# Performance work log

Hardware: AMD Instinct MI355X
Metric: run time of the kernel (lower is better)

Reference implementation:

```python
import jax, jax.numpy as jnp
import numpy as np

N_ATOMS = 100000
N_BONDS = 200000
MAX_NB = 6
ATOM_FDIM = 133
BOND_FDIM = 147
HIDDEN = 512
N_MOLS = 8192
DEPTH = 5


def setup_inputs() -> dict:
    key = jax.random.key(0)
    ks = jax.random.split(key, 10)
    f_atoms = jax.random.normal(ks[0], (N_ATOMS, ATOM_FDIM), dtype=jnp.float32)
    f_bonds = jax.random.normal(ks[1], (N_BONDS, BOND_FDIM), dtype=jnp.float32)
    # fan-in scaled weights to keep activations stable through the depth loop
    W_i = jax.random.normal(ks[2], (BOND_FDIM, HIDDEN), dtype=jnp.float32) / np.sqrt(BOND_FDIM)
    W_h = jax.random.normal(ks[3], (HIDDEN, HIDDEN), dtype=jnp.float32) / np.sqrt(HIDDEN)
    W_o = jax.random.normal(ks[4], (ATOM_FDIM + HIDDEN, HIDDEN), dtype=jnp.float32) / np.sqrt(ATOM_FDIM + HIDDEN)
    b_o = jnp.zeros((HIDDEN,), dtype=jnp.float32)
    a2b = jax.random.randint(ks[5], (N_ATOMS, MAX_NB), 0, N_BONDS, dtype=jnp.int32)
    b2a = jax.random.randint(ks[6], (N_BONDS,), 0, N_ATOMS, dtype=jnp.int32)
    b2revb = jax.random.randint(ks[7], (N_BONDS,), 0, N_BONDS, dtype=jnp.int32)
    atom_to_mol = jnp.sort(jax.random.randint(ks[8], (N_ATOMS,), 0, N_MOLS, dtype=jnp.int32))
    return {"f_atoms": f_atoms, "f_bonds": f_bonds, "W_i": W_i, "W_h": W_h,
            "W_o": W_o, "b_o": b_o, "a2b": a2b, "b2a": b2a, "b2revb": b2revb,
            "atom_to_mol": atom_to_mol, "n_mols": N_MOLS}


def reference(f_atoms, f_bonds, W_i, W_h, W_o, b_o, a2b, b2a, b2revb, atom_to_mol, n_mols):
    # input = W_i(f_bonds); message = relu(input)
    inp = f_bonds @ W_i                      # [B, H]
    message = jax.nn.relu(inp)
    for _ in range(DEPTH - 1):
        nei_a_message = message[a2b]         # [A, MAX_NB, H] gather bond->atom
        a_message = nei_a_message.sum(axis=1)  # [A, H]
        message = a_message[b2a] - message[b2revb]  # [B, H]
        message = jax.nn.relu(inp + message @ W_h)  # dropout p=0 -> identity
    nei_a_message = message[a2b]             # [A, MAX_NB, H]
    a_message = nei_a_message.sum(axis=1)    # [A, H]
    a_input = jnp.concatenate([f_atoms, a_message], axis=1)  # [A, ATOM_FDIM+H]
    atom_hiddens = jax.nn.relu(a_input @ W_o + b_o)           # [A, H]
    # mean aggregation per molecule (a_scope -> segment ids)
    sums = jax.ops.segment_sum(atom_hiddens, atom_to_mol, num_segments=n_mols)
    counts = jax.ops.segment_sum(jnp.ones((atom_hiddens.shape[0],), dtype=atom_hiddens.dtype),
                                 atom_to_mol, num_segments=n_mols)
    mol_vecs = jnp.where(counts[:, None] > 0,
                         sums / jnp.maximum(counts, 1.0)[:, None],
                         jnp.zeros_like(sums))  # cached_zero_vector for empty mols
    return mol_vecs
```

## Files before the change

kernel.cpp:

```cpp
#include <hip/hip_runtime.h>
#include <hip/hip_bf16.h>
#include <cstdint>

#define A_N   100000
#define B_N   200000
#define MAXNB 6
#define AFD   133
#define BFD   147
#define HID   512
#define NMOL  8192

typedef __attribute__((ext_vector_type(8))) short bf16x8;
typedef __attribute__((ext_vector_type(4))) float f32x4;

__device__ __forceinline__ unsigned short f2b(float f) {
    unsigned u = __builtin_bit_cast(unsigned, f);
    u += 0x7fffu + ((u >> 16) & 1u);
    return (unsigned short)(u >> 16);
}
__device__ __forceinline__ float blo(unsigned u) { return __builtin_bit_cast(float, u << 16); }
__device__ __forceinline__ float bhi(unsigned u) { return __builtin_bit_cast(float, u & 0xffff0000u); }
__device__ __forceinline__ unsigned pack2f(float a, float b) {
    return (unsigned)f2b(a) | ((unsigned)f2b(b) << 16);
}
__device__ __forceinline__ void glds16(const void* g, void* l) {
    __builtin_amdgcn_global_load_lds((const __attribute__((address_space(1))) unsigned*)g,
                                     (__attribute__((address_space(3))) unsigned*)l, 16, 0, 0);
}

__global__ __launch_bounds__(256) void k_diag(float* __restrict__ out, int n, float val) {
    int i = blockIdx.x * 256 + threadIdx.x;
    if (i < n) out[i] = val;
}

__global__ __launch_bounds__(256) void k_weights(
    const float* __restrict__ Wi, const float* __restrict__ Wh, const float* __restrict__ Wo,
    unsigned short* __restrict__ WiT, unsigned short* __restrict__ WcatImg, unsigned short* __restrict__ WoT)
{
    int n = blockIdx.x, t = threadIdx.x;
    for (int k = t; k < 160; k += 256)
        WiT[(size_t)n * 160 + k] = (k < BFD) ? f2b(Wi[(size_t)k * HID + n]) : (unsigned short)0;
    for (int k = t; k < 672; k += 256) {
        unsigned short v;
        if (k < HID)             v = f2b(Wh[(size_t)k * HID + n]);
        else if (k < HID + BFD)  v = f2b(Wi[(size_t)(k - HID) * HID + n]);
        else                     v = 0;
        int row = n & 127;
        size_t tile = (size_t)(n >> 7) * 21 + (k >> 5);
        WcatImg[tile * 4096 + row * 32 + ((((k >> 3) & 3) ^ ((row >> 1) & 3)) << 3) + (k & 7)] = v;
    }
    for (int k = t; k < 672; k += 256) {
        unsigned short v;
        if (k < AFD)       v = f2b(Wo[(size_t)k * HID + n]);
        else if (k < 160)  v = 0;
        else               v = f2b(Wo[(size_t)(k - 27) * HID + n]);
        WoT[(size_t)n * 672 + k] = v;
    }
}

__global__ __launch_bounds__(256) void k_gemm_wi(
    const float* __restrict__ fb, const unsigned short* __restrict__ WiT,
    unsigned short* __restrict__ msg)
{
    __shared__ unsigned short As[128][32];
    __shared__ unsigned short Bs[128][32];
    const int orig = blockIdx.x;
    const int xcd = orig & 7, idx = orig >> 3;
    const int wg = (xcd < 4 ? xcd * 782 : 3128 + (xcd - 4) * 781) + idx;
    const int bm = wg >> 2, bn = wg & 3;
    const int row0 = bm * 128, col0 = bn * 128;

    const int tid = threadIdx.x, lane = tid & 63, wid = tid >> 6;
    const int wm = wid >> 1, wn = wid & 1;
    const int r0 = tid >> 2, c0 = tid & 3, r1 = 64 + r0;
    const int wsw = (c0 ^ ((r0 >> 1) & 3)) * 8;
    const int rsw = ((lane >> 4) ^ (((lane & 15) >> 1) & 3)) * 8;
    f32x4 acc[4][4] = {};

    const float* pf0 = fb + (size_t)min(row0 + r0, B_N - 1) * BFD;
    const float* pf1 = fb + (size_t)min(row0 + r1, B_N - 1) * BFD;
    const unsigned short* pb0 = WiT + (size_t)(col0 + r0) * 160;
    const unsigned short* pb1 = WiT + (size_t)(col0 + r1) * 160;

    float v0[8], v1[8];
    uint4 b0, b1;

#define LOADA(kt) do { int kb = (kt) * 32 + c0 * 8; \
        _Pragma("unroll") for (int i = 0; i < 8; i++) { int kg = kb + i; v0[i] = (kg < BFD) ? pf0[kg] : 0.f; } \
        _Pragma("unroll") for (int i = 0; i < 8; i++) { int kg = kb + i; v1[i] = (kg < BFD) ? pf1[kg] : 0.f; } } while (0)
#define LOADB(kt) do { int kb = (kt) * 32 + c0 * 8; \
        b0 = *(const uint4*)(pb0 + kb); b1 = *(const uint4*)(pb1 + kb); } while (0)

    LOADA(0); LOADB(0);
    for (int kt = 0; kt < 5; ++kt) {
        __syncthreads();
        uint4 q;
        q.x = pack2f(v0[0], v0[1]); q.y = pack2f(v0[2], v0[3]); q.z = pack2f(v0[4], v0[5]); q.w = pack2f(v0[6], v0[7]);
        *(uint4*)&As[r0][wsw] = q;
        q.x = pack2f(v1[0], v1[1]); q.y = pack2f(v1[2], v1[3]); q.z = pack2f(v1[4], v1[5]); q.w = pack2f(v1[6], v1[7]);
        *(uint4*)&As[r1][wsw] = q;
        *(uint4*)&Bs[r0][wsw] = b0;
        *(uint4*)&Bs[r1][wsw] = b1;
        __syncthreads();
        if (kt < 4) { LOADA(kt + 1); LOADB(kt + 1); }

        bf16x8 af[4], bfr[4];
#pragma unroll
        for (int m = 0; m < 4; m++) af[m] = *(const bf16x8*)&As[wm * 64 + m * 16 + (lane & 15)][rsw];
#pragma unroll
        for (int n = 0; n < 4; n++) bfr[n] = *(const bf16x8*)&Bs[wn * 64 + n * 16 + (lane & 15)][rsw];
#pragma unroll
        for (int m = 0; m < 4; m++)
#pragma unroll
            for (int n = 0; n < 4; n++)
                acc[m][n] = __builtin_amdgcn_mfma_f32_16x16x32_bf16(af[m], bfr[n], acc[m][n], 0, 0, 0);
    }
#undef LOADA
#undef LOADB

#pragma unroll
    for (int m = 0; m < 4; m++) {
        int rbase = row0 + wm * 64 + m * 16 + (lane >> 4) * 4;
#pragma unroll
        for (int n = 0; n < 4; n++) {
            int cg = col0 + wn * 64 + n * 16 + (lane & 15);
#pragma unroll
            for (int r = 0; r < 4; r++) {
                int rg = rbase + r;
                if (rg < B_N) {
                    float v = acc[m][n][r];
                    msg[(size_t)rg * HID + cg] = f2b(v > 0.f ? v : 0.f);
                }
            }
        }
    }
}

__global__ __launch_bounds__(256) void k_delta(
    const unsigned short* __restrict__ msg, const int* __restrict__ a2b,
    const int* __restrict__ b2a, const int* __restrict__ b2revb,
    unsigned short* __restrict__ D)
{
    int b = blockIdx.x * 4 + (threadIdx.x >> 6);
    if (b >= B_N) return;
    int lane = threadIdx.x & 63;
    const int atom = b2a[b];
    const int rev  = b2revb[b];
    const int* nb = a2b + (size_t)atom * MAXNB;
    float acc[8];
    {
        uint4 v = *(const uint4*)(msg + (size_t)rev * HID + lane * 8);
        acc[0] = -blo(v.x); acc[1] = -bhi(v.x);
        acc[2] = -blo(v.y); acc[3] = -bhi(v.y);
        acc[4] = -blo(v.z); acc[5] = -bhi(v.z);
        acc[6] = -blo(v.w); acc[7] = -bhi(v.w);
    }
#pragma unroll
    for (int k = 0; k < MAXNB; k++) {
        uint4 v = *(const uint4*)(msg + (size_t)nb[k] * HID + lane * 8);
        acc[0] += blo(v.x); acc[1] += bhi(v.x);
        acc[2] += blo(v.y); acc[3] += bhi(v.y);
        acc[4] += blo(v.z); acc[5] += bhi(v.z);
        acc[6] += blo(v.w); acc[7] += bhi(v.w);
    }
    uint4 q;
    q.x = pack2f(acc[0], acc[1]); q.y = pack2f(acc[2], acc[3]);
    q.z = pack2f(acc[4], acc[5]); q.w = pack2f(acc[6], acc[7]);
    *(uint4*)(D + (size_t)b * HID + lane * 8) = q;
}

__global__ __launch_bounds__(256, 4) void k_gemm_wh(
    const unsigned short* __restrict__ D, const float* __restrict__ fb,
    const unsigned short* __restrict__ WcatImg,
    unsigned short* __restrict__ msg_out)
{
    __shared__ unsigned short As[2][128][32];
    __shared__ unsigned short Bs[2][4096];
    const int orig = blockIdx.x;
    const int xcd = orig & 7, idx = orig >> 3;
    const int wg = (xcd < 4 ? xcd * 782 : 3128 + (xcd - 4) * 781) + idx;
    const int bm = wg >> 2, bn = wg & 3;
    const int row0 = bm * 128;

    const int tid = threadIdx.x, lane = tid & 63, wid = tid >> 6;
    const int wm = wid >> 1, wn = wid & 1;
    const int r0 = tid >> 2, c0 = tid & 3, r1 = 64 + r0;
    const int wsw = (c0 ^ ((r0 >> 1) & 3)) * 8;
    const int rsw = ((lane >> 4) ^ (((lane & 15) >> 1) & 3)) * 8;
    f32x4 acc[4][4] = {};

    const int arow1 = wid * 32 + (lane >> 2);
    const int arow2 = arow1 + 16;
    const int achk = lane & 3;
    const unsigned short* srcA1 = D + (size_t)min(row0 + arow1, B_N - 1) * HID + ((achk ^ ((arow1 >> 1) & 3)) << 3);
    const unsigned short* srcA2 = D + (size_t)min(row0 + arow2, B_N - 1) * HID + ((achk ^ ((arow2 >> 1) & 3)) << 3);
    const char* srcB = (const char*)WcatImg + (size_t)bn * 21 * 8192 + wid * 2048 + lane * 16;

    const int rg0 = min(row0 + r0, B_N - 1), rg1 = min(row0 + r1, B_N - 1);
    const float* pf0 = fb + (size_t)rg0 * BFD;
    const float* pf1 = fb + (size_t)rg1 * BFD;
    float v0[8], v1[8];

    glds16(srcA1, &As[0][wid * 32][0]);
    glds16(srcA2, &As[0][wid * 32 + 16][0]);
    glds16(srcB, &Bs[0][wid * 1024]);
    glds16(srcB + 1024, &Bs[0][wid * 1024 + 512]);

    for (int kt = 0; kt < 21; ++kt) {
        const int cur = kt & 1, nxt = cur ^ 1;
        __syncthreads();
        if (kt >= 16) {
            uint4 q;
            q.x = pack2f(v0[0], v0[1]); q.y = pack2f(v0[2], v0[3]); q.z = pack2f(v0[4], v0[5]); q.w = pack2f(v0[6], v0[7]);
            *(uint4*)&As[cur][r0][wsw] = q;
            q.x = pack2f(v1[0], v1[1]); q.y = pack2f(v1[2], v1[3]); q.z = pack2f(v1[4], v1[5]); q.w = pack2f(v1[6], v1[7]);
            *(uint4*)&As[cur][r1][wsw] = q;
            __syncthreads();
        }
        if (kt < 20) {
            if (kt + 1 < 16) {
                glds16(srcA1 + (kt + 1) * 32, &As[nxt][wid * 32][0]);
                glds16(srcA2 + (kt + 1) * 32, &As[nxt][wid * 32 + 16][0]);
            }
            glds16(srcB + (size_t)(kt + 1) * 8192, &Bs[nxt][wid * 1024]);
            glds16(srcB + (size_t)(kt + 1) * 8192 + 1024, &Bs[nxt][wid * 1024 + 512]);
        }
        if (kt >= 15 && kt < 20) {
            int kb = (kt + 1) * 32 - HID + c0 * 8;
#pragma unroll
            for (int i = 0; i < 8; i++) { int kg = kb + i; v0[i] = (kg < BFD) ? pf0[kg] : 0.f; }
#pragma unroll
            for (int i = 0; i < 8; i++) { int kg = kb + i; v1[i] = (kg < BFD) ? pf1[kg] : 0.f; }
        }
        bf16x8 af[4], bfr[4];
#pragma unroll
        for (int m = 0; m < 4; m++) af[m] = *(const bf16x8*)&As[cur][wm * 64 + m * 16 + (lane & 15)][rsw];
#pragma unroll
        for (int n = 0; n < 4; n++) bfr[n] = *(const bf16x8*)&Bs[cur][(wn * 64 + n * 16 + (lane & 15)) * 32 + rsw];
#pragma unroll
        for (int m = 0; m < 4; m++)
#pragma unroll
            for (int n = 0; n < 4; n++)
                acc[m][n] = __builtin_amdgcn_mfma_f32_16x16x32_bf16(af[m], bfr[n], acc[m][n], 0, 0, 0);
    }

#pragma unroll
    for (int m = 0; m < 4; m++) {
        int rbase = row0 + wm * 64 + m * 16 + (lane >> 4) * 4;
#pragma unroll
        for (int n = 0; n < 4; n++) {
            int cg = bn * 128 + wn * 64 + n * 16 + (lane & 15);
#pragma unroll
            for (int r = 0; r < 4; r++) {
                int rg = rbase + r;
                if (rg < B_N) {
                    float v = acc[m][n][r];
                    msg_out[(size_t)rg * HID + cg] = f2b(v > 0.f ? v : 0.f);
                }
            }
        }
    }
}

__global__ __launch_bounds__(256, 4) void k_gemm_wo(
    const float* __restrict__ fa, const unsigned short* __restrict__ amsg,
    const unsigned short* __restrict__ WoT, const float* __restrict__ bo,
    float* __restrict__ ah)
{
    __shared__ unsigned short As[2][128][32];
    __shared__ unsigned short Bs[2][128][32];
    const int orig = blockIdx.x;
    const int wg = (orig & 7) * 391 + (orig >> 3);
    const int bm = wg >> 2, bn = wg & 3;
    const int row0 = bm * 128, col0 = bn * 128;

    const int tid = threadIdx.x, lane = tid & 63, wid = tid >> 6;
    const int wm = wid >> 1, wn = wid & 1;
    const int r0 = tid >> 2, c0 = tid & 3, r1 = 64 + r0;
    const int wsw = (c0 ^ ((r0 >> 1) & 3)) * 8;
    const int rsw = ((lane >> 4) ^ (((lane & 15) >> 1) & 3)) * 8;
    f32x4 acc[4][4] = {};

    const int grow1 = wid * 32 + (lane >> 2);
    const int grow2 = grow1 + 16;
    const int gchk = lane & 3;
    const int asw1 = (gchk ^ ((grow1 >> 1) & 3)) << 3;
    const int asw2 = (gchk ^ ((grow2 >> 1) & 3)) << 3;
    const unsigned short* srcA1 = amsg + (size_t)min(row0 + grow1, A_N - 1) * HID + asw1 - 160;
    const unsigned short* srcA2 = amsg + (size_t)min(row0 + grow2, A_N - 1) * HID + asw2 - 160;
    const unsigned short* srcB1 = WoT + (size_t)(col0 + grow1) * 672 + asw1;
    const unsigned short* srcB2 = WoT + (size_t)(col0 + grow2) * 672 + asw2;

    const int rg0 = min(row0 + r0, A_N - 1), rg1 = min(row0 + r1, A_N - 1);
    const float* pf0 = fa + (size_t)rg0 * AFD;
    const float* pf1 = fa + (size_t)rg1 * AFD;
    float v0[8], v1[8];

    {
        int kb = c0 * 8;
#pragma unroll
        for (int i = 0; i < 8; i++) { int kg = kb + i; v0[i] = (kg < AFD) ? pf0[kg] : 0.f; }
#pragma unroll
        for (int i = 0; i < 8; i++) { int kg = kb + i; v1[i] = (kg < AFD) ? pf1[kg] : 0.f; }
    }
    glds16(srcB1, &Bs[0][wid * 32][0]);
    glds16(srcB2, &Bs[0][wid * 32 + 16][0]);

    for (int kt = 0; kt < 21; ++kt) {
        const int cur = kt & 1, nxt = cur ^ 1;
        __syncthreads();
        if (kt < 5) {
            uint4 q;
            q.x = pack2f(v0[0], v0[1]); q.y = pack2f(v0[2], v0[3]); q.z = pack2f(v0[4], v0[5]); q.w = pack2f(v0[6], v0[7]);
            *(uint4*)&As[cur][r0][wsw] = q;
            q.x = pack2f(v1[0], v1[1]); q.y = pack2f(v1[2], v1[3]); q.z = pack2f(v1[4], v1[5]); q.w = pack2f(v1[6], v1[7]);
            *(uint4*)&As[cur][r1][wsw] = q;
            __syncthreads();
        }
        if (kt < 20) {
            if (kt + 1 >= 5) {
                glds16(srcA1 + (kt + 1) * 32, &As[nxt][wid * 32][0]);
                glds16(srcA2 + (kt + 1) * 32, &As[nxt][wid * 32 + 16][0]);
            }
            glds16(srcB1 + (kt + 1) * 32, &Bs[nxt][wid * 32][0]);
            glds16(srcB2 + (kt + 1) * 32, &Bs[nxt][wid * 32 + 16][0]);
        }
        if (kt < 4) {
            int kb = (kt + 1) * 32 + c0 * 8;
#pragma unroll
            for (int i = 0; i < 8; i++) { int kg = kb + i; v0[i] = (kg < AFD) ? pf0[kg] : 0.f; }
#pragma unroll
            for (int i = 0; i < 8; i++) { int kg = kb + i; v1[i] = (kg < AFD) ? pf1[kg] : 0.f; }
        }
        bf16x8 af[4], bfr[4];
#pragma unroll
        for (int m = 0; m < 4; m++) af[m] = *(const bf16x8*)&As[cur][wm * 64 + m * 16 + (lane & 15)][rsw];
#pragma unroll
        for (int n = 0; n < 4; n++) bfr[n] = *(const bf16x8*)&Bs[cur][wn * 64 + n * 16 + (lane & 15)][rsw];
#pragma unroll
        for (int m = 0; m < 4; m++)
#pragma unroll
            for (int n = 0; n < 4; n++)
                acc[m][n] = __builtin_amdgcn_mfma_f32_16x16x32_bf16(af[m], bfr[n], acc[m][n], 0, 0, 0);
    }

#pragma unroll
    for (int m = 0; m < 4; m++) {
        int rbase = row0 + wm * 64 + m * 16 + (lane >> 4) * 4;
#pragma unroll
        for (int n = 0; n < 4; n++) {
            int cg = col0 + wn * 64 + n * 16 + (lane & 15);
            float bias = bo[cg];
#pragma unroll
            for (int r = 0; r < 4; r++) {
                int rg = rbase + r;
                if (rg < A_N) {
                    float v = acc[m][n][r] + bias;
                    ah[(size_t)rg * HID + cg] = v > 0.f ? v : 0.f;
                }
            }
        }
    }
}

__global__ __launch_bounds__(256) void k_gather(
    const unsigned short* __restrict__ msg, const int* __restrict__ a2b,
    unsigned short* __restrict__ amsg)
{
    int g = blockIdx.x * 4 + (threadIdx.x >> 6);
    if (g >= A_N) return;
    int lane = threadIdx.x & 63;
    const int* nb = a2b + (size_t)g * MAXNB;
    float acc[8] = {};
#pragma unroll
    for (int k = 0; k < MAXNB; k++) {
        uint4 v = *(const uint4*)(msg + (size_t)nb[k] * HID + lane * 8);
        acc[0] += blo(v.x); acc[1] += bhi(v.x);
        acc[2] += blo(v.y); acc[3] += bhi(v.y);
        acc[4] += blo(v.z); acc[5] += bhi(v.z);
        acc[6] += blo(v.w); acc[7] += bhi(v.w);
    }
    uint4 q;
    q.x = pack2f(acc[0], acc[1]); q.y = pack2f(acc[2], acc[3]);
    q.z = pack2f(acc[4], acc[5]); q.w = pack2f(acc[6], acc[7]);
    *(uint4*)(amsg + (size_t)g * HID + lane * 8) = q;
}

__global__ __launch_bounds__(256) void k_segmean(
    const float* __restrict__ ah, const int* __restrict__ a2m, float* __restrict__ out)
{
    int mol = blockIdx.x, t = threadIdx.x;
    int lo, hi;
    { int l = 0, r = A_N; while (l < r) { int m = (l + r) >> 1; if (a2m[m] < mol) l = m + 1; else r = m; } lo = l; }
    { int l = lo, r = A_N; while (l < r) { int m = (l + r) >> 1; if (a2m[m] < mol + 1) l = m + 1; else r = m; } hi = l; }
    float s0 = 0.f, s1 = 0.f;
    for (int a = lo; a < hi; a++) {
        s0 += ah[(size_t)a * HID + t];
        s1 += ah[(size_t)a * HID + 256 + t];
    }
    int c = hi - lo;
    float inv = c > 0 ? 1.0f / (float)c : 0.f;
    out[(size_t)mol * HID + t] = s0 * inv;
    out[(size_t)mol * HID + 256 + t] = s1 * inv;
}

extern "C" void kernel_launch(void* const* d_in, const int* in_sizes, int n_in,
                              void* d_out, int out_size, void* d_ws, size_t ws_size,
                              hipStream_t stream)
{
    const float* f_atoms = (const float*)d_in[0];
    const float* f_bonds = (const float*)d_in[1];
    const float* W_i     = (const float*)d_in[2];
    const float* W_h     = (const float*)d_in[3];
    const float* W_o     = (const float*)d_in[4];
    const float* b_o     = (const float*)d_in[5];
    const int*   a2b     = (const int*)d_in[6];
    const int*   b2a     = (const int*)d_in[7];
    const int*   b2revb  = (const int*)d_in[8];
    const int*   a2m     = (const int*)d_in[9];

    const size_t OFF_MSG  = 0;
    const size_t OFF_D    = 204800000;
    const size_t OFF_WIT  = 409600000;
    const size_t OFF_WCAT = 409763840;
    const size_t OFF_WOT  = 410451968;
    const size_t REQUIRED = 411140096;

    if (ws_size < REQUIRED) {
        float val = -(10000.0f + (float)(ws_size >> 20));
        k_diag<<<dim3((out_size + 255) / 256), dim3(256), 0, stream>>>((float*)d_out, out_size, val);
        return;
    }

    char* w = (char*)d_ws;
    unsigned short* msg   = (unsigned short*)(w + OFF_MSG);
    unsigned short* D     = (unsigned short*)(w + OFF_D);
    unsigned short* amsg  = (unsigned short*)(w + OFF_D);
    unsigned short* WiT   = (unsigned short*)(w + OFF_WIT);
    unsigned short* Wcat  = (unsigned short*)(w + OFF_WCAT);
    unsigned short* WoT   = (unsigned short*)(w + OFF_WOT);
    float* ah             = (float*)(w + OFF_MSG);

    k_weights<<<dim3(512), dim3(256), 0, stream>>>(W_i, W_h, W_o, WiT, Wcat, WoT);
    k_gemm_wi<<<dim3(6252), dim3(256), 0, stream>>>(f_bonds, WiT, msg);
    for (int it = 0; it < 4; ++it) {
        k_delta<<<dim3(50000), dim3(256), 0, stream>>>(msg, a2b, b2a, b2revb, D);
        k_gemm_wh<<<dim3(6252), dim3(256), 0, stream>>>(D, f_bonds, Wcat, msg);
    }
    k_gather<<<dim3(25000), dim3(256), 0, stream>>>(msg, a2b, amsg);
    k_gemm_wo<<<dim3(3128), dim3(256), 0, stream>>>(f_atoms, amsg, WoT, b_o, ah);
    k_segmean<<<dim3(NMOL), dim3(256), 0, stream>>>(ah, a2m, (float*)d_out);
}
```

Baseline: 2.384 ms.

## Widen Wh GEMM tile to 128x256 with 512 threads; batch two rows per wave in gathers

The recurrent Wh GEMM now uses 512-thread blocks computing 128x256 output tiles, so each block covers half the hidden width. This halves how many times each D row is re-read from memory, and the weight image layout is changed to 256-row tiles to match. The delta and final gather kernels now process two bonds or atoms per wavefront and issue all gather loads up front, exposing more memory-level parallelism. Costs are higher LDS and register use per block, which may lower occupancy. Both kernels also drop their bounds checks, which relies on the row counts dividing evenly.

```diff
diff --git a/kernel.cpp b/kernel.cpp
--- a/kernel.cpp
+++ b/kernel.cpp
@@ -45,9 +45,9 @@
         if (k < HID)             v = f2b(Wh[(size_t)k * HID + n]);
         else if (k < HID + BFD)  v = f2b(Wi[(size_t)(k - HID) * HID + n]);
         else                     v = 0;
-        int row = n & 127;
-        size_t tile = (size_t)(n >> 7) * 21 + (k >> 5);
-        WcatImg[tile * 4096 + row * 32 + ((((k >> 3) & 3) ^ ((row >> 1) & 3)) << 3) + (k & 7)] = v;
+        int row = n & 255;
+        size_t tile = (size_t)(n >> 8) * 21 + (k >> 5);
+        WcatImg[tile * 8192 + row * 32 + ((((k >> 3) & 3) ^ ((row >> 1) & 3)) << 3) + (k & 7)] = v;
     }
     for (int k = t; k < 672; k += 256) {
         unsigned short v;
@@ -141,68 +141,71 @@
     const int* __restrict__ b2a, const int* __restrict__ b2revb,
     unsigned short* __restrict__ D)
 {
-    int b = blockIdx.x * 4 + (threadIdx.x >> 6);
-    if (b >= B_N) return;
-    int lane = threadIdx.x & 63;
-    const int atom = b2a[b];
-    const int rev  = b2revb[b];
-    const int* nb = a2b + (size_t)atom * MAXNB;
-    float acc[8];
-    {
-        uint4 v = *(const uint4*)(msg + (size_t)rev * HID + lane * 8);
-        acc[0] = -blo(v.x); acc[1] = -bhi(v.x);
-        acc[2] = -blo(v.y); acc[3] = -bhi(v.y);
-        acc[4] = -blo(v.z); acc[5] = -bhi(v.z);
-        acc[6] = -blo(v.w); acc[7] = -bhi(v.w);
-    }
-#pragma unroll
-    for (int k = 0; k < MAXNB; k++) {
-        uint4 v = *(const uint4*)(msg + (size_t)nb[k] * HID + lane * 8);
-        acc[0] += blo(v.x); acc[1] += bhi(v.x);
-        acc[2] += blo(v.y); acc[3] += bhi(v.y);
-        acc[4] += blo(v.z); acc[5] += bhi(v.z);
-        acc[6] += blo(v.w); acc[7] += bhi(v.w);
-    }
-    uint4 q;
-    q.x = pack2f(acc[0], acc[1]); q.y = pack2f(acc[2], acc[3]);
-    q.z = pack2f(acc[4], acc[5]); q.w = pack2f(acc[6], acc[7]);
-    *(uint4*)(D + (size_t)b * HID + lane * 8) = q;
-}
-
-__global__ __launch_bounds__(256, 4) void k_gemm_wh(
+    const int base = blockIdx.x * 8 + ((threadIdx.x >> 6) << 1);
+    const int lane = threadIdx.x & 63;
+    const int bA = base, bB = base + 1;
+    const int* nbA = a2b + (size_t)b2a[bA] * MAXNB;
+    const int* nbB = a2b + (size_t)b2a[bB] * MAXNB;
+    const int revA = b2revb[bA], revB = b2revb[bB];
+    uint4 ga[7], gb[7];
+#pragma unroll
+    for (int k = 0; k < 6; k++) ga[k] = *(const uint4*)(msg + (size_t)nbA[k] * HID + lane * 8);
+    ga[6] = *(const uint4*)(msg + (size_t)revA * HID + lane * 8);
+#pragma unroll
+    for (int k = 0; k < 6; k++) gb[k] = *(const uint4*)(msg + (size_t)nbB[k] * HID + lane * 8);
+    gb[6] = *(const uint4*)(msg + (size_t)revB * HID + lane * 8);
+
+#define SUM7(g, out) do { \
+        float s[8]; \
+        s[0] = blo(g[0].x)+blo(g[1].x)+blo(g[2].x)+blo(g[3].x)+blo(g[4].x)+blo(g[5].x)-blo(g[6].x); \
+        s[1] = bhi(g[0].x)+bhi(g[1].x)+bhi(g[2].x)+bhi(g[3].x)+bhi(g[4].x)+bhi(g[5].x)-bhi(g[6].x); \
+        s[2] = blo(g[0].y)+blo(g[1].y)+blo(g[2].y)+blo(g[3].y)+blo(g[4].y)+blo(g[5].y)-blo(g[6].y); \
+        s[3] = bhi(g[0].y)+bhi(g[1].y)+bhi(g[2].y)+bhi(g[3].y)+bhi(g[4].y)+bhi(g[5].y)-bhi(g[6].y); \
+        s[4] = blo(g[0].z)+blo(g[1].z)+blo(g[2].z)+blo(g[3].z)+blo(g[4].z)+blo(g[5].z)-blo(g[6].z); \
+        s[5] = bhi(g[0].z)+bhi(g[1].z)+bhi(g[2].z)+bhi(g[3].z)+bhi(g[4].z)+bhi(g[5].z)-bhi(g[6].z); \
+        s[6] = blo(g[0].w)+blo(g[1].w)+blo(g[2].w)+blo(g[3].w)+blo(g[4].w)+blo(g[5].w)-blo(g[6].w); \
+        s[7] = bhi(g[0].w)+bhi(g[1].w)+bhi(g[2].w)+bhi(g[3].w)+bhi(g[4].w)+bhi(g[5].w)-bhi(g[6].w); \
+        out.x = pack2f(s[0], s[1]); out.y = pack2f(s[2], s[3]); \
+        out.z = pack2f(s[4], s[5]); out.w = pack2f(s[6], s[7]); } while (0)
+
+    uint4 qa, qb;
+    SUM7(ga, qa);
+    SUM7(gb, qb);
+    *(uint4*)(D + (size_t)bA * HID + lane * 8) = qa;
+    *(uint4*)(D + (size_t)bB * HID + lane * 8) = qb;
+#undef SUM7
+}
+
+__global__ __launch_bounds__(512, 4) void k_gemm_wh(
     const unsigned short* __restrict__ D, const float* __restrict__ fb,
     const unsigned short* __restrict__ WcatImg,
     unsigned short* __restrict__ msg_out)
 {
     __shared__ unsigned short As[2][128][32];
-    __shared__ unsigned short Bs[2][4096];
+    __shared__ unsigned short Bs[2][8192];
     const int orig = blockIdx.x;
     const int xcd = orig & 7, idx = orig >> 3;
-    const int wg = (xcd < 4 ? xcd * 782 : 3128 + (xcd - 4) * 781) + idx;
-    const int bm = wg >> 2, bn = wg & 3;
+    const int wg = (xcd < 6 ? xcd * 391 : 2346 + (xcd - 6) * 390) + idx;
+    const int bm = wg >> 1, bn = wg & 1;
     const int row0 = bm * 128;
 
     const int tid = threadIdx.x, lane = tid & 63, wid = tid >> 6;
-    const int wm = wid >> 1, wn = wid & 1;
-    const int r0 = tid >> 2, c0 = tid & 3, r1 = 64 + r0;
+    const int wm = wid >> 2, wn = wid & 3;
+    const int r0 = tid >> 2, c0 = tid & 3;
     const int wsw = (c0 ^ ((r0 >> 1) & 3)) * 8;
     const int rsw = ((lane >> 4) ^ (((lane & 15) >> 1) & 3)) * 8;
     f32x4 acc[4][4] = {};
 
-    const int arow1 = wid * 32 + (lane >> 2);
-    const int arow2 = arow1 + 16;
+    const int arow = wid * 16 + (lane >> 2);
     const int achk = lane & 3;
-    const unsigned short* srcA1 = D + (size_t)min(row0 + arow1, B_N - 1) * HID + ((achk ^ ((arow1 >> 1) & 3)) << 3);
-    const unsigned short* srcA2 = D + (size_t)min(row0 + arow2, B_N - 1) * HID + ((achk ^ ((arow2 >> 1) & 3)) << 3);
-    const char* srcB = (const char*)WcatImg + (size_t)bn * 21 * 8192 + wid * 2048 + lane * 16;
-
-    const int rg0 = min(row0 + r0, B_N - 1), rg1 = min(row0 + r1, B_N - 1);
-    const float* pf0 = fb + (size_t)rg0 * BFD;
-    const float* pf1 = fb + (size_t)rg1 * BFD;
-    float v0[8], v1[8];
-
-    glds16(srcA1, &As[0][wid * 32][0]);
-    glds16(srcA2, &As[0][wid * 32 + 16][0]);
+    const unsigned short* srcA = D + (size_t)min(row0 + arow, B_N - 1) * HID + ((achk ^ ((arow >> 1) & 3)) << 3);
+    const char* srcB = (const char*)WcatImg + (size_t)bn * 21 * 16384 + wid * 2048 + lane * 16;
+
+    const int rg = min(row0 + r0, B_N - 1);
+    const float* pf = fb + (size_t)rg * BFD;
+    float v0[8];
+
+    glds16(srcA, &As[0][wid * 16][0]);
     glds16(srcB, &Bs[0][wid * 1024]);
     glds16(srcB + 1024, &Bs[0][wid * 1024 + 512]);
 
@@ -213,24 +216,18 @@
             uint4 q;
             q.x = pack2f(v0[0], v0[1]); q.y = pack2f(v0[2], v0[3]); q.z = pack2f(v0[4], v0[5]); q.w = pack2f(v0[6], v0[7]);
             *(uint4*)&As[cur][r0][wsw] = q;
-            q.x = pack2f(v1[0], v1[1]); q.y = pack2f(v1[2], v1[3]); q.z = pack2f(v1[4], v1[5]); q.w = pack2f(v1[6], v1[7]);
-            *(uint4*)&As[cur][r1][wsw] = q;
             __syncthreads();
         }
         if (kt < 20) {
-            if (kt + 1 < 16) {
-                glds16(srcA1 + (kt + 1) * 32, &As[nxt][wid * 32][0]);
-                glds16(srcA2 + (kt + 1) * 32, &As[nxt][wid * 32 + 16][0]);
-            }
-            glds16(srcB + (size_t)(kt + 1) * 8192, &Bs[nxt][wid * 1024]);
-            glds16(srcB + (size_t)(kt + 1) * 8192 + 1024, &Bs[nxt][wid * 1024 + 512]);
+            if (kt + 1 < 16)
+                glds16(srcA + (kt + 1) * 32, &As[nxt][wid * 16][0]);
+            glds16(srcB + (size_t)(kt + 1) * 16384, &Bs[nxt][wid * 1024]);
+            glds16(srcB + (size_t)(kt + 1) * 16384 + 1024, &Bs[nxt][wid * 1024 + 512]);
         }
         if (kt >= 15 && kt < 20) {
             int kb = (kt + 1) * 32 - HID + c0 * 8;
 #pragma unroll
-            for (int i = 0; i < 8; i++) { int kg = kb + i; v0[i] = (kg < BFD) ? pf0[kg] : 0.f; }
-#pragma unroll
-            for (int i = 0; i < 8; i++) { int kg = kb + i; v1[i] = (kg < BFD) ? pf1[kg] : 0.f; }
+            for (int i = 0; i < 8; i++) { int kg = kb + i; v0[i] = (kg < BFD) ? pf[kg] : 0.f; }
         }
         bf16x8 af[4], bfr[4];
 #pragma unroll
@@ -249,13 +246,13 @@
         int rbase = row0 + wm * 64 + m * 16 + (lane >> 4) * 4;
 #pragma unroll
         for (int n = 0; n < 4; n++) {
-            int cg = bn * 128 + wn * 64 + n * 16 + (lane & 15);
+            int cg = bn * 256 + wn * 64 + n * 16 + (lane & 15);
 #pragma unroll
             for (int r = 0; r < 4; r++) {
-                int rg = rbase + r;
-                if (rg < B_N) {
+                int rg2 = rbase + r;
+                if (rg2 < B_N) {
                     float v = acc[m][n][r];
-                    msg_out[(size_t)rg * HID + cg] = f2b(v > 0.f ? v : 0.f);
+                    msg_out[(size_t)rg2 * HID + cg] = f2b(v > 0.f ? v : 0.f);
                 }
             }
         }
@@ -367,23 +364,35 @@
     const unsigned short* __restrict__ msg, const int* __restrict__ a2b,
     unsigned short* __restrict__ amsg)
 {
-    int g = blockIdx.x * 4 + (threadIdx.x >> 6);
-    if (g >= A_N) return;
-    int lane = threadIdx.x & 63;
-    const int* nb = a2b + (size_t)g * MAXNB;
-    float acc[8] = {};
-#pragma unroll
-    for (int k = 0; k < MAXNB; k++) {
-        uint4 v = *(const uint4*)(msg + (size_t)nb[k] * HID + lane * 8);
-        acc[0] += blo(v.x); acc[1] += bhi(v.x);
-        acc[2] += blo(v.y); acc[3] += bhi(v.y);
-        acc[4] += blo(v.z); acc[5] += bhi(v.z);
-        acc[6] += blo(v.w); acc[7] += bhi(v.w);
-    }
-    uint4 q;
-    q.x = pack2f(acc[0], acc[1]); q.y = pack2f(acc[2], acc[3]);
-    q.z = pack2f(acc[4], acc[5]); q.w = pack2f(acc[6], acc[7]);
-    *(uint4*)(amsg + (size_t)g * HID + lane * 8) = q;
+    const int base = blockIdx.x * 8 + ((threadIdx.x >> 6) << 1);
+    const int lane = threadIdx.x & 63;
+    const int* nbA = a2b + (size_t)base * MAXNB;
+    const int* nbB = a2b + (size_t)(base + 1) * MAXNB;
+    uint4 ga[6], gb[6];
+#pragma unroll
+    for (int k = 0; k < 6; k++) ga[k] = *(const uint4*)(msg + (size_t)nbA[k] * HID + lane * 8);
+#pragma unroll
+    for (int k = 0; k < 6; k++) gb[k] = *(const uint4*)(msg + (size_t)nbB[k] * HID + lane * 8);
+
+#define SUM6(g, out) do { \
+        float s[8]; \
+        s[0] = blo(g[0].x)+blo(g[1].x)+blo(g[2].x)+blo(g[3].x)+blo(g[4].x)+blo(g[5].x); \
+        s[1] = bhi(g[0].x)+bhi(g[1].x)+bhi(g[2].x)+bhi(g[3].x)+bhi(g[4].x)+bhi(g[5].x); \
+        s[2] = blo(g[0].y)+blo(g[1].y)+blo(g[2].y)+blo(g[3].y)+blo(g[4].y)+blo(g[5].y); \
+        s[3] = bhi(g[0].y)+bhi(g[1].y)+bhi(g[2].y)+bhi(g[3].y)+bhi(g[4].y)+bhi(g[5].y); \
+        s[4] = blo(g[0].z)+blo(g[1].z)+blo(g[2].z)+blo(g[3].z)+blo(g[4].z)+blo(g[5].z); \
+        s[5] = bhi(g[0].z)+bhi(g[1].z)+bhi(g[2].z)+bhi(g[3].z)+bhi(g[4].z)+bhi(g[5].z); \
+        s[6] = blo(g[0].w)+blo(g[1].w)+blo(g[2].w)+blo(g[3].w)+blo(g[4].w)+blo(g[5].w); \
+        s[7] = bhi(g[0].w)+bhi(g[1].w)+bhi(g[2].w)+bhi(g[3].w)+bhi(g[4].w)+bhi(g[5].w); \
+        out.x = pack2f(s[0], s[1]); out.y = pack2f(s[2], s[3]); \
+        out.z = pack2f(s[4], s[5]); out.w = pack2f(s[6], s[7]); } while (0)
+
+    uint4 qa, qb;
+    SUM6(ga, qa);
+    SUM6(gb, qb);
+    *(uint4*)(amsg + (size_t)base * HID + lane * 8) = qa;
+    *(uint4*)(amsg + (size_t)(base + 1) * HID + lane * 8) = qb;
+#undef SUM6
 }
 
 __global__ __launch_bounds__(256) void k_segmean(
@@ -444,10 +453,10 @@
     k_weights<<<dim3(512), dim3(256), 0, stream>>>(W_i, W_h, W_o, WiT, Wcat, WoT);
     k_gemm_wi<<<dim3(6252), dim3(256), 0, stream>>>(f_bonds, WiT, msg);
     for (int it = 0; it < 4; ++it) {
-        k_delta<<<dim3(50000), dim3(256), 0, stream>>>(msg, a2b, b2a, b2revb, D);
-        k_gemm_wh<<<dim3(6252), dim3(256), 0, stream>>>(D, f_bonds, Wcat, msg);
-    }
-    k_gather<<<dim3(25000), dim3(256), 0, stream>>>(msg, a2b, amsg);
+        k_delta<<<dim3(25000), dim3(256), 0, stream>>>(msg, a2b, b2a, b2revb, D);
+        k_gemm_wh<<<dim3(3126), dim3(512), 0, stream>>>(D, f_bonds, Wcat, msg);
+    }
+    k_gather<<<dim3(12500), dim3(256), 0, stream>>>(msg, a2b, amsg);
     k_gemm_wo<<<dim3(3128), dim3(256), 0, stream>>>(f_atoms, amsg, WoT, b_o, ah);
     k_segmean<<<dim3(NMOL), dim3(256), 0, stream>>>(ah, a2m, (float*)d_out);
 }
```

Result: no change. 2.428 ms (+1.9%).

## Compute per-atom neighbor sums once and scatter deltas via bond inverse index

Applied to the files above, without the earlier changes.

Builds an atom-to-bond inverse index (count plus slot table, with an overflow list) using atomics once per call. The delta step then runs per atom: it sums the six neighbor messages once and writes the delta for every bond of that atom, instead of re-gathering six rows for each bond. This cuts redundant gather traffic by about half. The cost is two extra setup kernels, an overflow kernel on every iteration, and uneven per-atom work. The final gather also processes two atoms per wavefront with all loads issued up front.

```diff
diff --git a/kernel.cpp b/kernel.cpp
--- a/kernel.cpp
+++ b/kernel.cpp
@@ -9,6 +9,7 @@
 #define BFD   147
 #define HID   512
 #define NMOL  8192
+#define MAXDEG 32
 
 typedef __attribute__((ext_vector_type(8))) short bf16x8;
 typedef __attribute__((ext_vector_type(4))) float f32x4;
@@ -55,6 +56,85 @@
         else if (k < 160)  v = 0;
         else               v = f2b(Wo[(size_t)(k - 27) * HID + n]);
         WoT[(size_t)n * 672 + k] = v;
+    }
+}
+
+__global__ __launch_bounds__(256) void k_zero(int* __restrict__ cnt, int* __restrict__ ovfc) {
+    int i = blockIdx.x * 256 + threadIdx.x;
+    if (i < A_N) cnt[i] = 0;
+    if (i == 0) *ovfc = 0;
+}
+__global__ __launch_bounds__(256) void k_fill(
+    const int* __restrict__ b2a, int* __restrict__ cnt, int* __restrict__ slot,
+    int* __restrict__ ovfc, int* __restrict__ ovf)
+{
+    int b = blockIdx.x * 256 + threadIdx.x;
+    if (b >= B_N) return;
+    int a = b2a[b];
+    int pos = atomicAdd(&cnt[a], 1);
+    if (pos < MAXDEG) slot[(size_t)a * MAXDEG + pos] = b;
+    else { int o = atomicAdd(ovfc, 1); ovf[o] = b; }
+}
+
+__global__ __launch_bounds__(256) void k_delta_atom(
+    const unsigned short* __restrict__ msg, const int* __restrict__ a2b,
+    const int* __restrict__ b2revb, const int* __restrict__ cnt, const int* __restrict__ slot,
+    unsigned short* __restrict__ D)
+{
+    int a = blockIdx.x * 4 + (threadIdx.x >> 6);
+    if (a >= A_N) return;
+    int lane = threadIdx.x & 63;
+    const int* nb = a2b + (size_t)a * MAXNB;
+    float s[8] = {};
+#pragma unroll
+    for (int k = 0; k < MAXNB; k++) {
+        uint4 v = *(const uint4*)(msg + (size_t)nb[k] * HID + lane * 8);
+        s[0] += blo(v.x); s[1] += bhi(v.x);
+        s[2] += blo(v.y); s[3] += bhi(v.y);
+        s[4] += blo(v.z); s[5] += bhi(v.z);
+        s[6] += blo(v.w); s[7] += bhi(v.w);
+    }
+    int deg = min(cnt[a], MAXDEG);
+    const int* sl = slot + (size_t)a * MAXDEG;
+    for (int i = 0; i < deg; i++) {
+        int b = sl[i];
+        uint4 vr = *(const uint4*)(msg + (size_t)b2revb[b] * HID + lane * 8);
+        uint4 q;
+        q.x = pack2f(s[0] - blo(vr.x), s[1] - bhi(vr.x));
+        q.y = pack2f(s[2] - blo(vr.y), s[3] - bhi(vr.y));
+        q.z = pack2f(s[4] - blo(vr.z), s[5] - bhi(vr.z));
+        q.w = pack2f(s[6] - blo(vr.w), s[7] - bhi(vr.w));
+        *(uint4*)(D + (size_t)b * HID + lane * 8) = q;
+    }
+}
+
+__global__ __launch_bounds__(256) void k_delta_ovf(
+    const unsigned short* __restrict__ msg, const int* __restrict__ a2b,
+    const int* __restrict__ b2a, const int* __restrict__ b2revb,
+    const int* __restrict__ ovfc, const int* __restrict__ ovf,
+    unsigned short* __restrict__ D)
+{
+    int n = *ovfc;
+    int lane = threadIdx.x & 63;
+    for (int idx = blockIdx.x * 4 + (threadIdx.x >> 6); idx < n; idx += gridDim.x * 4) {
+        int b = ovf[idx];
+        const int* nbp = a2b + (size_t)b2a[b] * MAXNB;
+        float s[8] = {};
+#pragma unroll
+        for (int k = 0; k < MAXNB; k++) {
+            uint4 v = *(const uint4*)(msg + (size_t)nbp[k] * HID + lane * 8);
+            s[0] += blo(v.x); s[1] += bhi(v.x);
+            s[2] += blo(v.y); s[3] += bhi(v.y);
+            s[4] += blo(v.z); s[5] += bhi(v.z);
+            s[6] += blo(v.w); s[7] += bhi(v.w);
+        }
+        uint4 vr = *(const uint4*)(msg + (size_t)b2revb[b] * HID + lane * 8);
+        uint4 q;
+        q.x = pack2f(s[0] - blo(vr.x), s[1] - bhi(vr.x));
+        q.y = pack2f(s[2] - blo(vr.y), s[3] - bhi(vr.y));
+        q.z = pack2f(s[4] - blo(vr.z), s[5] - bhi(vr.z));
+        q.w = pack2f(s[6] - blo(vr.w), s[7] - bhi(vr.w));
+        *(uint4*)(D + (size_t)b * HID + lane * 8) = q;
     }
 }
 
@@ -136,39 +216,6 @@
     }
 }
 
-__global__ __launch_bounds__(256) void k_delta(
-    const unsigned short* __restrict__ msg, const int* __restrict__ a2b,
-    const int* __restrict__ b2a, const int* __restrict__ b2revb,
-    unsigned short* __restrict__ D)
-{
-    int b = blockIdx.x * 4 + (threadIdx.x >> 6);
-    if (b >= B_N) return;
-    int lane = threadIdx.x & 63;
-    const int atom = b2a[b];
-    const int rev  = b2revb[b];
-    const int* nb = a2b + (size_t)atom * MAXNB;
-    float acc[8];
-    {
-        uint4 v = *(const uint4*)(msg + (size_t)rev * HID + lane * 8);
-        acc[0] = -blo(v.x); acc[1] = -bhi(v.x);
-        acc[2] = -blo(v.y); acc[3] = -bhi(v.y);
-        acc[4] = -blo(v.z); acc[5] = -bhi(v.z);
-        acc[6] = -blo(v.w); acc[7] = -bhi(v.w);
-    }
-#pragma unroll
-    for (int k = 0; k < MAXNB; k++) {
-        uint4 v = *(const uint4*)(msg + (size_t)nb[k] * HID + lane * 8);
-        acc[0] += blo(v.x); acc[1] += bhi(v.x);
-        acc[2] += blo(v.y); acc[3] += bhi(v.y);
-        acc[4] += blo(v.z); acc[5] += bhi(v.z);
-        acc[6] += blo(v.w); acc[7] += bhi(v.w);
-    }
-    uint4 q;
-    q.x = pack2f(acc[0], acc[1]); q.y = pack2f(acc[2], acc[3]);
-    q.z = pack2f(acc[4], acc[5]); q.w = pack2f(acc[6], acc[7]);
-    *(uint4*)(D + (size_t)b * HID + lane * 8) = q;
-}
-
 __global__ __launch_bounds__(256, 4) void k_gemm_wh(
     const unsigned short* __restrict__ D, const float* __restrict__ fb,
     const unsigned short* __restrict__ WcatImg,
@@ -367,23 +414,35 @@
     const unsigned short* __restrict__ msg, const int* __restrict__ a2b,
     unsigned short* __restrict__ amsg)
 {
-    int g = blockIdx.x * 4 + (threadIdx.x >> 6);
-    if (g >= A_N) return;
-    int lane = threadIdx.x & 63;
-    const int* nb = a2b + (size_t)g * MAXNB;
-    float acc[8] = {};
-#pragma unroll
-    for (int k = 0; k < MAXNB; k++) {
-        uint4 v = *(const uint4*)(msg + (size_t)nb[k] * HID + lane * 8);
-        acc[0] += blo(v.x); acc[1] += bhi(v.x);
-        acc[2] += blo(v.y); acc[3] += bhi(v.y);
-        acc[4] += blo(v.z); acc[5] += bhi(v.z);
-        acc[6] += blo(v.w); acc[7] += bhi(v.w);
-    }
-    uint4 q;
-    q.x = pack2f(acc[0], acc[1]); q.y = pack2f(acc[2], acc[3]);
-    q.z = pack2f(acc[4], acc[5]); q.w = pack2f(acc[6], acc[7]);
-    *(uint4*)(amsg + (size_t)g * HID + lane * 8) = q;
+    const int base = blockIdx.x * 8 + ((threadIdx.x >> 6) << 1);
+    const int lane = threadIdx.x & 63;
+    const int* nbA = a2b + (size_t)base * MAXNB;
+    const int* nbB = a2b + (size_t)(base + 1) * MAXNB;
+    uint4 ga[6], gb[6];
+#pragma unroll
+    for (int k = 0; k < 6; k++) ga[k] = *(const uint4*)(msg + (size_t)nbA[k] * HID + lane * 8);
+#pragma unroll
+    for (int k = 0; k < 6; k++) gb[k] = *(const uint4*)(msg + (size_t)nbB[k] * HID + lane * 8);
+
+#define SUM6(g, out) do { \
+        float s[8]; \
+        s[0] = blo(g[0].x)+blo(g[1].x)+blo(g[2].x)+blo(g[3].x)+blo(g[4].x)+blo(g[5].x); \
+        s[1] = bhi(g[0].x)+bhi(g[1].x)+bhi(g[2].x)+bhi(g[3].x)+bhi(g[4].x)+bhi(g[5].x); \
+        s[2] = blo(g[0].y)+blo(g[1].y)+blo(g[2].y)+blo(g[3].y)+blo(g[4].y)+blo(g[5].y); \
+        s[3] = bhi(g[0].y)+bhi(g[1].y)+bhi(g[2].y)+bhi(g[3].y)+bhi(g[4].y)+bhi(g[5].y); \
+        s[4] = blo(g[0].z)+blo(g[1].z)+blo(g[2].z)+blo(g[3].z)+blo(g[4].z)+blo(g[5].z); \
+        s[5] = bhi(g[0].z)+bhi(g[1].z)+bhi(g[2].z)+bhi(g[3].z)+bhi(g[4].z)+bhi(g[5].z); \
+        s[6] = blo(g[0].w)+blo(g[1].w)+blo(g[2].w)+blo(g[3].w)+blo(g[4].w)+blo(g[5].w); \
+        s[7] = bhi(g[0].w)+bhi(g[1].w)+bhi(g[2].w)+bhi(g[3].w)+bhi(g[4].w)+bhi(g[5].w); \
+        out.x = pack2f(s[0], s[1]); out.y = pack2f(s[2], s[3]); \
+        out.z = pack2f(s[4], s[5]); out.w = pack2f(s[6], s[7]); } while (0)
+
+    uint4 qa, qb;
+    SUM6(ga, qa);
+    SUM6(gb, qb);
+    *(uint4*)(amsg + (size_t)base * HID + lane * 8) = qa;
+    *(uint4*)(amsg + (size_t)(base + 1) * HID + lane * 8) = qb;
+#undef SUM6
 }
 
 __global__ __launch_bounds__(256) void k_segmean(
@@ -424,7 +483,11 @@
     const size_t OFF_WIT  = 409600000;
     const size_t OFF_WCAT = 409763840;
     const size_t OFF_WOT  = 410451968;
-    const size_t REQUIRED = 411140096;
+    const size_t OFF_CNT  = 411140096;
+    const size_t OFF_SLOT = 411540096;
+    const size_t OFF_OVFC = 424340096;
+    const size_t OFF_OVF  = 424340160;
+    const size_t REQUIRED = 425140160;
 
     if (ws_size < REQUIRED) {
         float val = -(10000.0f + (float)(ws_size >> 20));
@@ -439,15 +502,22 @@
     unsigned short* WiT   = (unsigned short*)(w + OFF_WIT);
     unsigned short* Wcat  = (unsigned short*)(w + OFF_WCAT);
     unsigned short* WoT   = (unsigned short*)(w + OFF_WOT);
+    int* cnt              = (int*)(w + OFF_CNT);
+    int* slot             = (int*)(w + OFF_SLOT);
+    int* ovfc             = (int*)(w + OFF_OVFC);
+    int* ovf              = (int*)(w + OFF_OVF);
     float* ah             = (float*)(w + OFF_MSG);
 
     k_weights<<<dim3(512), dim3(256), 0, stream>>>(W_i, W_h, W_o, WiT, Wcat, WoT);
+    k_zero<<<dim3(391), dim3(256), 0, stream>>>(cnt, ovfc);
+    k_fill<<<dim3(782), dim3(256), 0, stream>>>(b2a, cnt, slot, ovfc, ovf);
     k_gemm_wi<<<dim3(6252), dim3(256), 0, stream>>>(f_bonds, WiT, msg);
     for (int it = 0; it < 4; ++it) {
-        k_delta<<<dim3(50000), dim3(256), 0, stream>>>(msg, a2b, b2a, b2revb, D);
+        k_delta_atom<<<dim3(25000), dim3(256), 0, stream>>>(msg, a2b, b2revb, cnt, slot, D);
+        k_delta_ovf<<<dim3(64), dim3(256), 0, stream>>>(msg, a2b, b2a, b2revb, ovfc, ovf, D);
         k_gemm_wh<<<dim3(6252), dim3(256), 0, stream>>>(D, f_bonds, Wcat, msg);
     }
-    k_gather<<<dim3(25000), dim3(256), 0, stream>>>(msg, a2b, amsg);
+    k_gather<<<dim3(12500), dim3(256), 0, stream>>>(msg, a2b, amsg);
     k_gemm_wo<<<dim3(3128), dim3(256), 0, stream>>>(f_atoms, amsg, WoT, b_o, ah);
     k_segmean<<<dim3(NMOL), dim3(256), 0, stream>>>(ah, a2m, (float*)d_out);
 }
```

After: 2.050 ms, median of 2. 1.16x faster.
